# Kernel optimization log

Measured on AMD Instinct MI355X. Metric: run time of the kernel, lower is better.

Reference implementation:

```python
import jax, jax.numpy as jnp
import numpy as np

N = 50000          # nodes
E = 640000         # edges (before self-loops)
DIM_FEATS = 128
DIM_H = 32
HEADS1 = 8
NUM_CLASS = 16
NEG_SLOPE_ATT = 0.2   # PyG GATv2Conv default negative_slope
NEG_SLOPE_OUT = 0.01  # F.leaky_relu default


def setup_inputs() -> dict:
    key = jax.random.key(0)
    ks = jax.random.split(key, 12)
    s = 0.1
    x = jax.random.normal(ks[0], (N, DIM_FEATS), dtype=jnp.float32)
    edge_index = jax.random.randint(ks[1], (2, E), 0, N, dtype=jnp.int32)
    # GATv2Conv layer 1: dim_feats -> dim_h per head, 8 heads, concat
    W1l = jax.random.normal(ks[2], (DIM_FEATS, HEADS1 * DIM_H), dtype=jnp.float32) * s
    W1r = jax.random.normal(ks[3], (DIM_FEATS, HEADS1 * DIM_H), dtype=jnp.float32) * s
    att1 = jax.random.normal(ks[4], (HEADS1, DIM_H), dtype=jnp.float32) * s
    b1 = jnp.zeros((HEADS1 * DIM_H,), dtype=jnp.float32)
    # GATv2Conv layer 2: 256 -> num_class, 1 head, concat=False
    W2l = jax.random.normal(ks[5], (HEADS1 * DIM_H, NUM_CLASS), dtype=jnp.float32) * s
    W2r = jax.random.normal(ks[6], (HEADS1 * DIM_H, NUM_CLASS), dtype=jnp.float32) * s
    att2 = jax.random.normal(ks[7], (1, NUM_CLASS), dtype=jnp.float32) * s
    b2 = jnp.zeros((NUM_CLASS,), dtype=jnp.float32)
    return {"x": x, "edge_index": edge_index, "W1l": W1l, "W1r": W1r,
            "att1": att1, "b1": b1, "W2l": W2l, "W2r": W2r,
            "att2": att2, "b2": b2}


def _segment_softmax(scores, seg, num_segments):
    # scores: [E, H], seg: [E] destination node ids
    m = jax.ops.segment_max(scores, seg, num_segments=num_segments)  # [N, H]
    e = jnp.exp(scores - m[seg])
    denom = jax.ops.segment_sum(e, seg, num_segments=num_segments)   # [N, H]
    return e / (denom[seg] + 1e-16)


def _gatv2_layer(x, src, dst, Wl, Wr, att, bias, heads, out_ch, concat):
    n = x.shape[0]
    xl = (x @ Wl).reshape(n, heads, out_ch)  # source transform
    xr = (x @ Wr).reshape(n, heads, out_ch)  # target transform
    # per-edge GATv2 score: a^T LeakyReLU(xl[j] + xr[i])
    e = jax.nn.leaky_relu(xl[src] + xr[dst], negative_slope=NEG_SLOPE_ATT)  # [E,H,F]
    alpha = jnp.einsum('ehf,hf->eh', e, att)                                # [E,H]
    alpha = _segment_softmax(alpha, dst, n)
    msg = xl[src] * alpha[:, :, None]                                       # [E,H,F]
    out = jax.ops.segment_sum(msg, dst, num_segments=n)                     # [N,H,F]
    out = out.reshape(n, heads * out_ch) if concat else out.mean(axis=1)
    return out + bias


def reference(x, edge_index, W1l, W1r, att1, b1, W2l, W2r, att2, b2):
    # add_self_loops=True (PyG GATv2Conv default)
    loop = jnp.arange(N, dtype=edge_index.dtype)
    src = jnp.concatenate([edge_index[0], loop])
    dst = jnp.concatenate([edge_index[1], loop])
    # eval mode: all dropouts are identity
    h = _gatv2_layer(x, src, dst, W1l, W1r, att1, b1, HEADS1, DIM_H, concat=True)
    h = jax.nn.elu(h)
    h = _gatv2_layer(h, src, dst, W2l, W2r, att2, b2, 1, NUM_CLASS, concat=False)
    return jax.nn.leaky_relu(h, negative_slope=NEG_SLOPE_OUT)
```

## Files before the change

### kernel.cpp

```cpp
#include <hip/hip_runtime.h>
#include <math.h>

#define NN 50000
#define E0 640000
#define ET 690000
#define F1 128
#define D1 256
#define C2 16
#define NB 196
#define MPAD 50048
#define PADK 136
#define PADK2 264
#define LOG2E 1.4426950408889634f
#define NBK1 782

typedef _Float16 f16x8 __attribute__((ext_vector_type(8)));
typedef _Float16 h2 __attribute__((ext_vector_type(2)));
typedef __attribute__((ext_vector_type(4))) float f32x4;

__device__ __forceinline__ unsigned short f2h(float f) {
  union { _Float16 h; unsigned short u; } c;
  c.h = (_Float16)f;
  return c.u;
}
__device__ __forceinline__ float h2f(unsigned short u) {
  union { unsigned short u; _Float16 h; } c; c.u = u; return (float)c.h;
}
__device__ __forceinline__ h2 u2h2(unsigned u) {
  union { unsigned u; h2 h; } c; c.u = u; return c.h;
}
__device__ __forceinline__ unsigned h22u(h2 h) {
  union { h2 h; unsigned u; } c; c.h = h; return c.u;
}

__global__ __launch_bounds__(256) void k_prep(
    const float* __restrict__ x, const float* __restrict__ Wl,
    const float* __restrict__ Wr, const float* __restrict__ W2l,
    const float* __restrict__ W2r, const int* __restrict__ ei,
    unsigned short* __restrict__ xb, unsigned short* __restrict__ wt,
    unsigned short* __restrict__ wt2, int* __restrict__ deg) {
  const int b = blockIdx.x;
  if (b < 6256) {
    long long i = (long long)(b * 256 + threadIdx.x) * 4;
    if (i >= (long long)MPAD * F1) return;
    float4 v = (i < (long long)NN * F1) ? *(const float4*)&x[i]
                                        : make_float4(0.f, 0.f, 0.f, 0.f);
    ushort4 o;
    o.x = f2h(v.x); o.y = f2h(v.y); o.z = f2h(v.z); o.w = f2h(v.w);
    *(ushort4*)&xb[i] = o;
  } else if (b < 6512) {
    int tid = (b - 6256) * 256 + threadIdx.x;
    int n = tid >> 7, k = tid & 127;
    float v = (n < 256) ? Wl[k * 256 + n] : Wr[k * 256 + (n - 256)];
    wt[tid] = f2h(v);
  } else if (b < 6544) {
    int tid = (b - 6512) * 256 + threadIdx.x;
    int n = tid >> 8, k = tid & 255;
    float v = (n < 16) ? W2l[k * 16 + n] : W2r[k * 16 + (n - 16)];
    wt2[tid] = f2h(v);
  } else {
    int e = (b - 6544) * 256 + threadIdx.x;
    if (e >= ET) return;
    int d = (e < E0) ? ei[E0 + e] : (e - E0);
    atomicAdd(&deg[d], 1);
  }
}

__global__ __launch_bounds__(256) void k_gemm1m(
    const unsigned short* __restrict__ xb, const unsigned short* __restrict__ wt,
    unsigned short* __restrict__ xlh, unsigned short* __restrict__ xrh) {
  __shared__ unsigned short Al[128 * PADK];
  __shared__ unsigned short Bl[128 * PADK];
  const int t = threadIdx.x;
  const int m0 = blockIdx.x * 128;
  const int n0 = blockIdx.y * 128;
  {
    const int r = t >> 4;
    const int c = (t & 15) * 8;
#pragma unroll
    for (int p = 0; p < 8; ++p) {
      const int row = r + p * 16;
      *(float4*)&Al[row * PADK + c] = *(const float4*)&xb[(size_t)(m0 + row) * F1 + c];
      *(float4*)&Bl[row * PADK + c] = *(const float4*)&wt[(size_t)(n0 + row) * F1 + c];
    }
  }
  __syncthreads();
  const int wave = t >> 6, lane = t & 63;
  const int mw = (wave >> 1) * 64, nw = (wave & 1) * 64;
  const int fr = lane & 15, fq = lane >> 4;
  f32x4 acc[4][4] = {};
#pragma unroll
  for (int ks = 0; ks < 4; ++ks) {
    const int ko = ks * 32 + fq * 8;
    f16x8 a[4], b[4];
#pragma unroll
    for (int i = 0; i < 4; ++i)
      a[i] = *(const f16x8*)&Al[(mw + i * 16 + fr) * PADK + ko];
#pragma unroll
    for (int j = 0; j < 4; ++j)
      b[j] = *(const f16x8*)&Bl[(nw + j * 16 + fr) * PADK + ko];
#pragma unroll
    for (int i = 0; i < 4; ++i)
#pragma unroll
      for (int j = 0; j < 4; ++j)
        acc[i][j] = __builtin_amdgcn_mfma_f32_16x16x32_f16(a[i], b[j], acc[i][j], 0, 0, 0);
  }
  unsigned short* outp = (n0 < 256) ? xlh : xrh;
  const int cb = (n0 & 255) + nw + fr;
#pragma unroll
  for (int j = 0; j < 4; ++j) {
    const int col = cb + j * 16;
    const int head = col >> 5, f = col & 31;
    unsigned short* hp = outp + (size_t)head * NN * 32 + f;
#pragma unroll
    for (int i = 0; i < 4; ++i) {
      const int gm0 = m0 + mw + i * 16 + fq * 4;
#pragma unroll
      for (int r = 0; r < 4; ++r) {
        const int gm = gm0 + r;
        if (gm < NN) hp[(size_t)gm * 32] = f2h(acc[i][j][r]);
      }
    }
  }
}

__global__ __launch_bounds__(256) void k_scan_part(const int* __restrict__ deg,
                                                   int* __restrict__ part) {
  int i = blockIdx.x * 256 + threadIdx.x;
  int v = (i < NN) ? deg[i] : 0;
  v += __shfl_xor(v, 1);  v += __shfl_xor(v, 2);  v += __shfl_xor(v, 4);
  v += __shfl_xor(v, 8);  v += __shfl_xor(v, 16); v += __shfl_xor(v, 32);
  __shared__ int w[4];
  if ((threadIdx.x & 63) == 0) w[threadIdx.x >> 6] = v;
  __syncthreads();
  if (threadIdx.x == 0) part[blockIdx.x] = w[0] + w[1] + w[2] + w[3];
}

__global__ __launch_bounds__(256) void k_scan_top(int* __restrict__ part,
                                                  int* __restrict__ offs) {
  __shared__ int lds[256];
  int t = threadIdx.x;
  int v = (t < NB) ? part[t] : 0;
  lds[t] = v;
  __syncthreads();
  for (int off = 1; off < 256; off <<= 1) {
    int u = (t >= off) ? lds[t - off] : 0;
    __syncthreads();
    lds[t] += u;
    __syncthreads();
  }
  if (t < NB) part[t] = lds[t] - v;
  if (t == 255) offs[NN] = lds[255];
}

__global__ __launch_bounds__(256) void k_scan_apply(int* __restrict__ deg,
                                                    const int* __restrict__ part,
                                                    int* __restrict__ offs) {
  __shared__ int lds[256];
  int t = threadIdx.x;
  int i = blockIdx.x * 256 + t;
  int v = (i < NN) ? deg[i] : 0;
  lds[t] = v;
  __syncthreads();
  for (int off = 1; off < 256; off <<= 1) {
    int u = (t >= off) ? lds[t - off] : 0;
    __syncthreads();
    lds[t] += u;
    __syncthreads();
  }
  int excl = lds[t] - v + part[blockIdx.x];
  if (i < NN) { offs[i] = excl; deg[i] = excl; }
}

__global__ void k_scatter(const int* __restrict__ ei, int* __restrict__ cur,
                          unsigned short* __restrict__ csr) {
  int e = blockIdx.x * 256 + threadIdx.x;
  if (e >= ET) return;
  int s, d;
  if (e < E0) { s = ei[e]; d = ei[E0 + e]; } else { s = d = e - E0; }
  int pos = atomicAdd(&cur[d], 1);
  csr[pos] = (unsigned short)s;
}

__global__ __launch_bounds__(256) void k_agg1(
    const unsigned short* __restrict__ xlh, const unsigned short* __restrict__ xrh,
    unsigned short* __restrict__ hb,
    const int* __restrict__ offs, const unsigned short* __restrict__ csr,
    const float* __restrict__ att, const float* __restrict__ b1) {
  const int b = blockIdx.x;
  const int head = b & 7;
  const int wave = threadIdx.x >> 6;
  const int lane = threadIdx.x & 63;
  const int g = lane >> 2;
  const int j4 = lane & 3;
  const int n = (b >> 3) * 64 + wave * 16 + g;
  const bool valid = n < NN;
  const int colh = j4 * 8;
  const int col = head * 32 + colh;
  const unsigned short* xlhead = xlh + (size_t)head * NN * 32;

  const int nc = valid ? n : 0;
  const uint4 xru = *(const uint4*)&xrh[((size_t)head * NN + nc) * 32 + colh];
  h2 xr2[4];
  xr2[0] = u2h2(xru.x); xr2[1] = u2h2(xru.y);
  xr2[2] = u2h2(xru.z); xr2[3] = u2h2(xru.w);
  float at8[8];
  *(float4*)&at8[0] = *(const float4*)&att[col];
  *(float4*)&at8[4] = *(const float4*)&att[col + 4];
  h2 ath6[4], ath4[4];
#pragma unroll
  for (int j = 0; j < 4; ++j) {
    ath6[j] = h2{(_Float16)(at8[2 * j] * (0.6f * LOG2E)),
                 (_Float16)(at8[2 * j + 1] * (0.6f * LOG2E))};
    ath4[j] = h2{(_Float16)(at8[2 * j] * (0.4f * LOG2E)),
                 (_Float16)(at8[2 * j + 1] * (0.4f * LOG2E))};
  }
  float l = 0.f;
  h2 acc2[4] = {h2{0, 0}, h2{0, 0}, h2{0, 0}, h2{0, 0}};
  const int beg = valid ? offs[n] : 0;
  const int fin = valid ? offs[n + 1] : 0;

  auto score = [&](const h2* xh) -> float {
    float cv = 0.f, ca = 0.f;
#pragma unroll
    for (int j = 0; j < 4; ++j) {
      h2 v = xh[j] + xr2[j];
      h2 a = u2h2(h22u(v) & 0x7FFF7FFFu);
      cv = __builtin_amdgcn_fdot2(v, ath6[j], cv, false);
      ca = __builtin_amdgcn_fdot2(a, ath4[j], ca, false);
    }
    float c = cv + ca;
    c += __shfl_xor(c, 1);
    c += __shfl_xor(c, 2);
    return c;
  };

  int idx = beg;
  for (; idx + 1 < fin; idx += 2) {
    const int s0 = csr[idx], s1 = csr[idx + 1];
    const uint4 w0 = *(const uint4*)&xlhead[(size_t)s0 * 32 + colh];
    const uint4 w1 = *(const uint4*)&xlhead[(size_t)s1 * 32 + colh];
    h2 xh0[4], xh1[4];
    xh0[0] = u2h2(w0.x); xh0[1] = u2h2(w0.y); xh0[2] = u2h2(w0.z); xh0[3] = u2h2(w0.w);
    xh1[0] = u2h2(w1.x); xh1[1] = u2h2(w1.y); xh1[2] = u2h2(w1.z); xh1[3] = u2h2(w1.w);
    const float c0 = score(xh0);
    const float c1 = score(xh1);
    const float p0 = exp2f(c0), p1 = exp2f(c1);
    l += p0 + p1;
    const _Float16 p0h = (_Float16)p0, p1h = (_Float16)p1;
    const h2 p02 = h2{p0h, p0h}, p12 = h2{p1h, p1h};
#pragma unroll
    for (int j = 0; j < 4; ++j) acc2[j] += p02 * xh0[j] + p12 * xh1[j];
  }
  if (idx < fin) {
    const int s0 = csr[idx];
    const uint4 w0 = *(const uint4*)&xlhead[(size_t)s0 * 32 + colh];
    h2 xh0[4];
    xh0[0] = u2h2(w0.x); xh0[1] = u2h2(w0.y); xh0[2] = u2h2(w0.z); xh0[3] = u2h2(w0.w);
    const float c0 = score(xh0);
    const float p0 = exp2f(c0);
    l += p0;
    const _Float16 p0h = (_Float16)p0;
    const h2 p02 = h2{p0h, p0h};
#pragma unroll
    for (int j = 0; j < 4; ++j) acc2[j] += p02 * xh0[j];
  }
  if (valid) {
    const float rl = 1.f / (l + 1e-16f);
    float b8[8], o[8];
    *(float4*)&b8[0] = *(const float4*)&b1[col];
    *(float4*)&b8[4] = *(const float4*)&b1[col + 4];
#pragma unroll
    for (int j = 0; j < 4; ++j) {
      o[2 * j]     = (float)acc2[j][0] * rl + b8[2 * j];
      o[2 * j + 1] = (float)acc2[j][1] * rl + b8[2 * j + 1];
    }
#pragma unroll
    for (int k = 0; k < 8; ++k) o[k] = o[k] > 0.f ? o[k] : expm1f(o[k]);
    ushort4 p;
    p.x = f2h(o[0]); p.y = f2h(o[1]); p.z = f2h(o[2]); p.w = f2h(o[3]);
    ushort4 q;
    q.x = f2h(o[4]); q.y = f2h(o[5]); q.z = f2h(o[6]); q.w = f2h(o[7]);
    uint4 packed;
    packed.x = *(unsigned*)&p.x; packed.y = *(unsigned*)&p.z;
    packed.z = *(unsigned*)&q.x; packed.w = *(unsigned*)&q.z;
    *(uint4*)&hb[(size_t)n * D1 + col] = packed;
  }
}

__global__ __launch_bounds__(256) void k_gemm2m(
    const unsigned short* __restrict__ hb, const unsigned short* __restrict__ wt2,
    unsigned short* __restrict__ h2lh, float* __restrict__ h2r) {
  __shared__ unsigned short Bl[32 * PADK2];
  const int t = threadIdx.x;
  {
    const int n = t >> 3, k0 = (t & 7) * 32;
#pragma unroll
    for (int j = 0; j < 4; ++j)
      *(uint4*)&Bl[n * PADK2 + k0 + j * 8] = *(const uint4*)&wt2[n * 256 + k0 + j * 8];
  }
  __syncthreads();
  const int wave = t >> 6, lane = t & 63;
  const int fr = lane & 15, fq = lane >> 4;
  const int m0 = blockIdx.x * 128 + wave * 32;
  f32x4 acc[2][2] = {};
#pragma unroll
  for (int ks = 0; ks < 8; ++ks) {
    const int ko = ks * 32 + fq * 8;
    f16x8 a[2], b[2];
#pragma unroll
    for (int i = 0; i < 2; ++i) {
      int row = m0 + i * 16 + fr; if (row >= NN) row = NN - 1;
      a[i] = *(const f16x8*)&hb[(size_t)row * D1 + ko];
    }
#pragma unroll
    for (int j = 0; j < 2; ++j)
      b[j] = *(const f16x8*)&Bl[(j * 16 + fr) * PADK2 + ko];
#pragma unroll
    for (int i = 0; i < 2; ++i)
#pragma unroll
      for (int j = 0; j < 2; ++j)
        acc[i][j] = __builtin_amdgcn_mfma_f32_16x16x32_f16(a[i], b[j], acc[i][j], 0, 0, 0);
  }
#pragma unroll
  for (int i = 0; i < 2; ++i) {
    const int gm0 = m0 + i * 16 + fq * 4;
#pragma unroll
    for (int r = 0; r < 4; ++r) {
      const int gm = gm0 + r;
      if (gm < NN) {
        h2lh[(size_t)gm * C2 + fr] = f2h(acc[i][0][r]);
        h2r[(size_t)gm * C2 + fr] = acc[i][1][r];
      }
    }
  }
}

__global__ __launch_bounds__(256) void k_agg2(
    const unsigned short* __restrict__ h2lh, const float* __restrict__ h2r,
    const int* __restrict__ offs, const unsigned short* __restrict__ csr,
    const float* __restrict__ att2, const float* __restrict__ b2,
    float* __restrict__ out) {
  const int wave = threadIdx.x >> 6;
  const int lane = threadIdx.x & 63;
  const int n = blockIdx.x * 4 + wave;
  if (n >= NN) return;
  const int c = lane & 15, g = lane >> 4;
  const float xr_v = h2r[(size_t)n * C2 + c];
  const float att_v = att2[c] * LOG2E;
  float l = 0.f, acc = 0.f;
  const int beg = offs[n], fin = offs[n + 1];
  for (int idx = beg + g; idx < fin; idx += 4) {
    int s = csr[idx];
    float xlv = h2f(h2lh[(size_t)s * C2 + c]);
    float v = xlv + xr_v;
    v = fmaxf(v, 0.2f * v);
    float sc0 = v * att_v;
    sc0 += __shfl_xor(sc0, 1);
    sc0 += __shfl_xor(sc0, 2);
    sc0 += __shfl_xor(sc0, 4);
    sc0 += __shfl_xor(sc0, 8);
    float p = exp2f(sc0);
    l += p;
    acc = fmaf(p, xlv, acc);
  }
  l += __shfl_xor(l, 16);   l += __shfl_xor(l, 32);
  acc += __shfl_xor(acc, 16); acc += __shfl_xor(acc, 32);
  float o = acc / (l + 1e-16f) + b2[c];
  o = o > 0.f ? o : 0.01f * o;
  if (lane < 16) out[(size_t)n * C2 + c] = o;
}

extern "C" void kernel_launch(void* const* d_in, const int* in_sizes, int n_in,
                              void* d_out, int out_size, void* d_ws, size_t ws_size,
                              hipStream_t stream) {
  const float* x    = (const float*)d_in[0];
  const int*   ei   = (const int*)d_in[1];
  const float* W1l  = (const float*)d_in[2];
  const float* W1r  = (const float*)d_in[3];
  const float* att1 = (const float*)d_in[4];
  const float* b1   = (const float*)d_in[5];
  const float* W2l  = (const float*)d_in[6];
  const float* W2r  = (const float*)d_in[7];
  const float* att2 = (const float*)d_in[8];
  const float* b2   = (const float*)d_in[9];
  float* out = (float*)d_out;

  unsigned short* xlh = (unsigned short*)d_ws;
  unsigned short* xrh = xlh + (size_t)NN * D1;
  unsigned short* hb  = xrh + (size_t)NN * D1;
  int* deg  = (int*)(hb + (size_t)NN * D1);
  int* offs = deg + NN;
  unsigned short* csr = (unsigned short*)(offs + NN + 1);
  int* part = (int*)(csr + ET + 2);
  unsigned short* xb = (unsigned short*)(part + NB);
  unsigned short* wt = xb + (size_t)MPAD * F1;
  unsigned short* wt2 = wt + 512 * F1;
  unsigned short* h2lh = xlh;
  float* h2r = (float*)(h2lh + (size_t)NN * C2);

  hipMemsetAsync(deg, 0, NN * sizeof(int), stream);
  k_prep<<<6544 + (ET + 255) / 256, 256, 0, stream>>>(
      x, W1l, W1r, W2l, W2r, ei, xb, wt, wt2, deg);
  k_gemm1m<<<dim3(MPAD / 128, 4), 256, 0, stream>>>(xb, wt, xlh, xrh);
  k_scan_part<<<NB, 256, 0, stream>>>(deg, part);
  k_scan_top<<<1, 256, 0, stream>>>(part, offs);
  k_scan_apply<<<NB, 256, 0, stream>>>(deg, part, offs);
  k_scatter<<<(ET + 255) / 256, 256, 0, stream>>>(ei, deg, csr);
  k_agg1<<<NBK1 * 8, 256, 0, stream>>>(xlh, xrh, hb, offs, csr, att1, b1);
  k_gemm2m<<<(NN + 127) / 128, 256, 0, stream>>>(hb, wt2, h2lh, h2r);
  k_agg2<<<NN / 4, 256, 0, stream>>>(h2lh, h2r, offs, csr, att2, b2, out);
}
```

Measured before the change: 271.9 us.

## Fuse CSR build into one persistent kernel with grid barriers, fold x cast into GEMM

After: 465.1 us. 1.71x slower.

```diff
diff --git a/kernel.cpp b/kernel.cpp
--- a/kernel.cpp
+++ b/kernel.cpp
@@ -7,12 +7,12 @@
 #define F1 128
 #define D1 256
 #define C2 16
-#define NB 196
 #define MPAD 50048
 #define PADK 136
-#define PADK2 264
 #define LOG2E 1.4426950408889634f
 #define NBK1 782
+#define CSRB 512
+#define CH 98
 
 typedef _Float16 f16x8 __attribute__((ext_vector_type(8)));
 typedef _Float16 h2 __attribute__((ext_vector_type(2)));
@@ -33,41 +33,84 @@
   union { h2 h; unsigned u; } c; c.h = h; return c.u;
 }
 
-__global__ __launch_bounds__(256) void k_prep(
-    const float* __restrict__ x, const float* __restrict__ Wl,
-    const float* __restrict__ Wr, const float* __restrict__ W2l,
-    const float* __restrict__ W2r, const int* __restrict__ ei,
-    unsigned short* __restrict__ xb, unsigned short* __restrict__ wt,
-    unsigned short* __restrict__ wt2, int* __restrict__ deg) {
-  const int b = blockIdx.x;
-  if (b < 6256) {
-    long long i = (long long)(b * 256 + threadIdx.x) * 4;
-    if (i >= (long long)MPAD * F1) return;
-    float4 v = (i < (long long)NN * F1) ? *(const float4*)&x[i]
-                                        : make_float4(0.f, 0.f, 0.f, 0.f);
-    ushort4 o;
-    o.x = f2h(v.x); o.y = f2h(v.y); o.z = f2h(v.z); o.w = f2h(v.w);
-    *(ushort4*)&xb[i] = o;
-  } else if (b < 6512) {
-    int tid = (b - 6256) * 256 + threadIdx.x;
-    int n = tid >> 7, k = tid & 127;
-    float v = (n < 256) ? Wl[k * 256 + n] : Wr[k * 256 + (n - 256)];
-    wt[tid] = f2h(v);
-  } else if (b < 6544) {
-    int tid = (b - 6512) * 256 + threadIdx.x;
-    int n = tid >> 8, k = tid & 255;
-    float v = (n < 16) ? W2l[k * 16 + n] : W2r[k * 16 + (n - 16)];
-    wt2[tid] = f2h(v);
-  } else {
-    int e = (b - 6544) * 256 + threadIdx.x;
-    if (e >= ET) return;
+__device__ __forceinline__ void gbar(int* bar, int target) {
+  __syncthreads();
+  if (threadIdx.x == 0) {
+    __threadfence();
+    atomicAdd(bar, 1);
+    while (__hip_atomic_load(bar, __ATOMIC_RELAXED, __HIP_MEMORY_SCOPE_AGENT) < target)
+      __builtin_amdgcn_s_sleep(1);
+  }
+  __syncthreads();
+  __threadfence();
+}
+
+__global__ __launch_bounds__(256) void k_csr(
+    const float* __restrict__ Wl, const float* __restrict__ Wr,
+    const float* __restrict__ W2l, const float* __restrict__ W2r,
+    const int* __restrict__ ei,
+    unsigned short* __restrict__ wt, unsigned short* __restrict__ wt2,
+    int* __restrict__ deg, int* __restrict__ offs,
+    unsigned short* __restrict__ csr, int* __restrict__ part,
+    int* __restrict__ bar) {
+  const int b = blockIdx.x, t = threadIdx.x;
+  const int gtid = b * 256 + t;
+  for (int i = gtid; i < 512 * 128 + 32 * 256; i += CSRB * 256) {
+    if (i < 512 * 128) {
+      int n = i >> 7, k = i & 127;
+      wt[i] = f2h((n < 256) ? Wl[k * 256 + n] : Wr[k * 256 + (n - 256)]);
+    } else {
+      int j = i - 512 * 128;
+      int n = j >> 8, k = j & 255;
+      wt2[j] = f2h((n < 16) ? W2l[k * 16 + n] : W2r[k * 16 + (n - 16)]);
+    }
+  }
+  for (int e = gtid; e < ET; e += CSRB * 256) {
     int d = (e < E0) ? ei[E0 + e] : (e - E0);
     atomicAdd(&deg[d], 1);
   }
+  gbar(bar, CSRB);
+  __shared__ int lds[128];
+  __shared__ int red[5];
+  const int base = b * CH;
+  const int i0 = base + t;
+  int v = (t < CH && i0 < NN) ? deg[i0] : 0;
+  if (t < 128) lds[t] = v;
+  __syncthreads();
+  for (int off = 1; off < 128; off <<= 1) {
+    int u = (t >= off && t < 128) ? lds[t - off] : 0;
+    __syncthreads();
+    if (t < 128) lds[t] += u;
+    __syncthreads();
+  }
+  const int sumb = lds[127];
+  if (t == 0) part[b] = sumb;
+  gbar(bar, 2 * CSRB);
+  int pp = 0;
+  for (int i = t; i < b; i += 256)
+    pp += __hip_atomic_load(&part[i], __ATOMIC_RELAXED, __HIP_MEMORY_SCOPE_AGENT);
+  pp += __shfl_xor(pp, 1);  pp += __shfl_xor(pp, 2);  pp += __shfl_xor(pp, 4);
+  pp += __shfl_xor(pp, 8);  pp += __shfl_xor(pp, 16); pp += __shfl_xor(pp, 32);
+  if ((t & 63) == 0) red[t >> 6] = pp;
+  __syncthreads();
+  const int prefix = red[0] + red[1] + red[2] + red[3];
+  if (t < CH && i0 < NN) {
+    int excl = prefix + lds[t] - v;
+    offs[i0] = excl;
+    deg[i0] = excl;
+  }
+  if (b == CSRB - 1 && t == 0) offs[NN] = prefix + sumb;
+  gbar(bar, 3 * CSRB);
+  for (int e = gtid; e < ET; e += CSRB * 256) {
+    int s, d;
+    if (e < E0) { s = ei[e]; d = ei[E0 + e]; } else { s = d = e - E0; }
+    int pos = atomicAdd(&deg[d], 1);
+    csr[pos] = (unsigned short)s;
+  }
 }
 
 __global__ __launch_bounds__(256) void k_gemm1m(
-    const unsigned short* __restrict__ xb, const unsigned short* __restrict__ wt,
+    const float* __restrict__ x, const unsigned short* __restrict__ wt,
     unsigned short* __restrict__ xlh, unsigned short* __restrict__ xrh) {
   __shared__ unsigned short Al[128 * PADK];
   __shared__ unsigned short Bl[128 * PADK];
@@ -80,7 +123,16 @@
 #pragma unroll
     for (int p = 0; p < 8; ++p) {
       const int row = r + p * 16;
-      *(float4*)&Al[row * PADK + c] = *(const float4*)&xb[(size_t)(m0 + row) * F1 + c];
+      const int rg = m0 + row;
+      const float* xp = &x[(size_t)(rg < NN ? rg : NN - 1) * F1 + c];
+      float4 lo = *(const float4*)xp;
+      float4 hi = *(const float4*)(xp + 4);
+      h2 q0 = h2{(_Float16)lo.x, (_Float16)lo.y};
+      h2 q1 = h2{(_Float16)lo.z, (_Float16)lo.w};
+      h2 q2 = h2{(_Float16)hi.x, (_Float16)hi.y};
+      h2 q3 = h2{(_Float16)hi.z, (_Float16)hi.w};
+      uint4 st; st.x = h22u(q0); st.y = h22u(q1); st.z = h22u(q2); st.w = h22u(q3);
+      *(uint4*)&Al[row * PADK + c] = st;
       *(float4*)&Bl[row * PADK + c] = *(const float4*)&wt[(size_t)(n0 + row) * F1 + c];
     }
   }
@@ -122,64 +174,6 @@
       }
     }
   }
-}
-
-__global__ __launch_bounds__(256) void k_scan_part(const int* __restrict__ deg,
-                                                   int* __restrict__ part) {
-  int i = blockIdx.x * 256 + threadIdx.x;
-  int v = (i < NN) ? deg[i] : 0;
-  v += __shfl_xor(v, 1);  v += __shfl_xor(v, 2);  v += __shfl_xor(v, 4);
-  v += __shfl_xor(v, 8);  v += __shfl_xor(v, 16); v += __shfl_xor(v, 32);
-  __shared__ int w[4];
-  if ((threadIdx.x & 63) == 0) w[threadIdx.x >> 6] = v;
-  __syncthreads();
-  if (threadIdx.x == 0) part[blockIdx.x] = w[0] + w[1] + w[2] + w[3];
-}
-
-__global__ __launch_bounds__(256) void k_scan_top(int* __restrict__ part,
-                                                  int* __restrict__ offs) {
-  __shared__ int lds[256];
-  int t = threadIdx.x;
-  int v = (t < NB) ? part[t] : 0;
-  lds[t] = v;
-  __syncthreads();
-  for (int off = 1; off < 256; off <<= 1) {
-    int u = (t >= off) ? lds[t - off] : 0;
-    __syncthreads();
-    lds[t] += u;
-    __syncthreads();
-  }
-  if (t < NB) part[t] = lds[t] - v;
-  if (t == 255) offs[NN] = lds[255];
-}
-
-__global__ __launch_bounds__(256) void k_scan_apply(int* __restrict__ deg,
-                                                    const int* __restrict__ part,
-                                                    int* __restrict__ offs) {
-  __shared__ int lds[256];
-  int t = threadIdx.x;
-  int i = blockIdx.x * 256 + t;
-  int v = (i < NN) ? deg[i] : 0;
-  lds[t] = v;
-  __syncthreads();
-  for (int off = 1; off < 256; off <<= 1) {
-    int u = (t >= off) ? lds[t - off] : 0;
-    __syncthreads();
-    lds[t] += u;
-    __syncthreads();
-  }
-  int excl = lds[t] - v + part[blockIdx.x];
-  if (i < NN) { offs[i] = excl; deg[i] = excl; }
-}
-
-__global__ void k_scatter(const int* __restrict__ ei, int* __restrict__ cur,
-                          unsigned short* __restrict__ csr) {
-  int e = blockIdx.x * 256 + threadIdx.x;
-  if (e >= ET) return;
-  int s, d;
-  if (e < E0) { s = ei[e]; d = ei[E0 + e]; } else { s = d = e - E0; }
-  int pos = atomicAdd(&cur[d], 1);
-  csr[pos] = (unsigned short)s;
 }
 
 __global__ __launch_bounds__(256) void k_agg1(
@@ -291,15 +285,7 @@
 __global__ __launch_bounds__(256) void k_gemm2m(
     const unsigned short* __restrict__ hb, const unsigned short* __restrict__ wt2,
     unsigned short* __restrict__ h2lh, float* __restrict__ h2r) {
-  __shared__ unsigned short Bl[32 * PADK2];
   const int t = threadIdx.x;
-  {
-    const int n = t >> 3, k0 = (t & 7) * 32;
-#pragma unroll
-    for (int j = 0; j < 4; ++j)
-      *(uint4*)&Bl[n * PADK2 + k0 + j * 8] = *(const uint4*)&wt2[n * 256 + k0 + j * 8];
-  }
-  __syncthreads();
   const int wave = t >> 6, lane = t & 63;
   const int fr = lane & 15, fq = lane >> 4;
   const int m0 = blockIdx.x * 128 + wave * 32;
@@ -315,7 +301,7 @@
     }
 #pragma unroll
     for (int j = 0; j < 2; ++j)
-      b[j] = *(const f16x8*)&Bl[(j * 16 + fr) * PADK2 + ko];
+      b[j] = *(const f16x8*)&wt2[(j * 16 + fr) * 256 + ko];
 #pragma unroll
     for (int i = 0; i < 2; ++i)
 #pragma unroll
@@ -390,23 +376,19 @@
   unsigned short* xrh = xlh + (size_t)NN * D1;
   unsigned short* hb  = xrh + (size_t)NN * D1;
   int* deg  = (int*)(hb + (size_t)NN * D1);
-  int* offs = deg + NN;
+  int* part = deg + NN;
+  int* bar  = part + CSRB;
+  int* offs = bar + 1;
   unsigned short* csr = (unsigned short*)(offs + NN + 1);
-  int* part = (int*)(csr + ET + 2);
-  unsigned short* xb = (unsigned short*)(part + NB);
-  unsigned short* wt = xb + (size_t)MPAD * F1;
+  unsigned short* wt  = csr + ET + 2;
   unsigned short* wt2 = wt + 512 * F1;
   unsigned short* h2lh = xlh;
   float* h2r = (float*)(h2lh + (size_t)NN * C2);
 
-  hipMemsetAsync(deg, 0, NN * sizeof(int), stream);
-  k_prep<<<6544 + (ET + 255) / 256, 256, 0, stream>>>(
-      x, W1l, W1r, W2l, W2r, ei, xb, wt, wt2, deg);
-  k_gemm1m<<<dim3(MPAD / 128, 4), 256, 0, stream>>>(xb, wt, xlh, xrh);
-  k_scan_part<<<NB, 256, 0, stream>>>(deg, part);
-  k_scan_top<<<1, 256, 0, stream>>>(part, offs);
-  k_scan_apply<<<NB, 256, 0, stream>>>(deg, part, offs);
-  k_scatter<<<(ET + 255) / 256, 256, 0, stream>>>(ei, deg, csr);
+  hipMemsetAsync(deg, 0, (NN + CSRB + 1) * sizeof(int), stream);
+  k_csr<<<CSRB, 256, 0, stream>>>(W1l, W1r, W2l, W2r, ei, wt, wt2,
+                                  deg, offs, csr, part, bar);
+  k_gemm1m<<<dim3(MPAD / 128, 4), 256, 0, stream>>>(x, wt, xlh, xrh);
   k_agg1<<<NBK1 * 8, 256, 0, stream>>>(xlh, xrh, hb, offs, csr, att1, b1);
   k_gemm2m<<<(NN + 127) / 128, 256, 0, stream>>>(hb, wt2, h2lh, h2r);
   k_agg2<<<NN / 4, 256, 0, stream>>>(h2lh, h2r, offs, csr, att2, b2, out);
```

## Fuse x fp16 conversion into GEMM1, drop scan_top kernel and gemm2 LDS staging

Applied to the files above, without the earlier changes.

After: 270.2 us. Within noise of the previous version (-0.6%).

```diff
diff --git a/kernel.cpp b/kernel.cpp
--- a/kernel.cpp
+++ b/kernel.cpp
@@ -10,7 +10,6 @@
 #define NB 196
 #define MPAD 50048
 #define PADK 136
-#define PADK2 264
 #define LOG2E 1.4426950408889634f
 #define NBK1 782
 
@@ -34,32 +33,24 @@
 }
 
 __global__ __launch_bounds__(256) void k_prep(
-    const float* __restrict__ x, const float* __restrict__ Wl,
-    const float* __restrict__ Wr, const float* __restrict__ W2l,
-    const float* __restrict__ W2r, const int* __restrict__ ei,
-    unsigned short* __restrict__ xb, unsigned short* __restrict__ wt,
-    unsigned short* __restrict__ wt2, int* __restrict__ deg) {
+    const float* __restrict__ Wl, const float* __restrict__ Wr,
+    const float* __restrict__ W2l, const float* __restrict__ W2r,
+    const int* __restrict__ ei,
+    unsigned short* __restrict__ wt, unsigned short* __restrict__ wt2,
+    int* __restrict__ deg) {
   const int b = blockIdx.x;
-  if (b < 6256) {
-    long long i = (long long)(b * 256 + threadIdx.x) * 4;
-    if (i >= (long long)MPAD * F1) return;
-    float4 v = (i < (long long)NN * F1) ? *(const float4*)&x[i]
-                                        : make_float4(0.f, 0.f, 0.f, 0.f);
-    ushort4 o;
-    o.x = f2h(v.x); o.y = f2h(v.y); o.z = f2h(v.z); o.w = f2h(v.w);
-    *(ushort4*)&xb[i] = o;
-  } else if (b < 6512) {
-    int tid = (b - 6256) * 256 + threadIdx.x;
+  if (b < 256) {
+    int tid = b * 256 + threadIdx.x;
     int n = tid >> 7, k = tid & 127;
     float v = (n < 256) ? Wl[k * 256 + n] : Wr[k * 256 + (n - 256)];
     wt[tid] = f2h(v);
-  } else if (b < 6544) {
-    int tid = (b - 6512) * 256 + threadIdx.x;
+  } else if (b < 288) {
+    int tid = (b - 256) * 256 + threadIdx.x;
     int n = tid >> 8, k = tid & 255;
     float v = (n < 16) ? W2l[k * 16 + n] : W2r[k * 16 + (n - 16)];
     wt2[tid] = f2h(v);
   } else {
-    int e = (b - 6544) * 256 + threadIdx.x;
+    int e = (b - 288) * 256 + threadIdx.x;
     if (e >= ET) return;
     int d = (e < E0) ? ei[E0 + e] : (e - E0);
     atomicAdd(&deg[d], 1);
@@ -67,7 +58,7 @@
 }
 
 __global__ __launch_bounds__(256) void k_gemm1m(
-    const unsigned short* __restrict__ xb, const unsigned short* __restrict__ wt,
+    const float* __restrict__ x, const unsigned short* __restrict__ wt,
     unsigned short* __restrict__ xlh, unsigned short* __restrict__ xrh) {
   __shared__ unsigned short Al[128 * PADK];
   __shared__ unsigned short Bl[128 * PADK];
@@ -80,7 +71,16 @@
 #pragma unroll
     for (int p = 0; p < 8; ++p) {
       const int row = r + p * 16;
-      *(float4*)&Al[row * PADK + c] = *(const float4*)&xb[(size_t)(m0 + row) * F1 + c];
+      const int rg = m0 + row;
+      const float* xp = &x[(size_t)(rg < NN ? rg : NN - 1) * F1 + c];
+      float4 lo = *(const float4*)xp;
+      float4 hi = *(const float4*)(xp + 4);
+      h2 q0 = h2{(_Float16)lo.x, (_Float16)lo.y};
+      h2 q1 = h2{(_Float16)lo.z, (_Float16)lo.w};
+      h2 q2 = h2{(_Float16)hi.x, (_Float16)hi.y};
+      h2 q3 = h2{(_Float16)hi.z, (_Float16)hi.w};
+      uint4 st; st.x = h22u(q0); st.y = h22u(q1); st.z = h22u(q2); st.w = h22u(q3);
+      *(uint4*)&Al[row * PADK + c] = st;
       *(float4*)&Bl[row * PADK + c] = *(const float4*)&wt[(size_t)(n0 + row) * F1 + c];
     }
   }
@@ -136,40 +136,31 @@
   if (threadIdx.x == 0) part[blockIdx.x] = w[0] + w[1] + w[2] + w[3];
 }
 
-__global__ __launch_bounds__(256) void k_scan_top(int* __restrict__ part,
-                                                  int* __restrict__ offs) {
+__global__ __launch_bounds__(256) void k_scan_apply(int* __restrict__ deg,
+                                                    const int* __restrict__ part,
+                                                    int* __restrict__ offs) {
   __shared__ int lds[256];
-  int t = threadIdx.x;
-  int v = (t < NB) ? part[t] : 0;
+  __shared__ int red[4];
+  const int b = blockIdx.x, t = threadIdx.x;
+  const int i = b * 256 + t;
+  int v = (i < NN) ? deg[i] : 0;
   lds[t] = v;
+  int pp = 0;
+  for (int j = t; j < b; j += 256) pp += part[j];
+  pp += __shfl_xor(pp, 1);  pp += __shfl_xor(pp, 2);  pp += __shfl_xor(pp, 4);
+  pp += __shfl_xor(pp, 8);  pp += __shfl_xor(pp, 16); pp += __shfl_xor(pp, 32);
+  if ((t & 63) == 0) red[t >> 6] = pp;
   __syncthreads();
+  const int prefix = red[0] + red[1] + red[2] + red[3];
   for (int off = 1; off < 256; off <<= 1) {
     int u = (t >= off) ? lds[t - off] : 0;
     __syncthreads();
     lds[t] += u;
     __syncthreads();
   }
-  if (t < NB) part[t] = lds[t] - v;
-  if (t == 255) offs[NN] = lds[255];
-}
-
-__global__ __launch_bounds__(256) void k_scan_apply(int* __restrict__ deg,
-                                                    const int* __restrict__ part,
-                                                    int* __restrict__ offs) {
-  __shared__ int lds[256];
-  int t = threadIdx.x;
-  int i = blockIdx.x * 256 + t;
-  int v = (i < NN) ? deg[i] : 0;
-  lds[t] = v;
-  __syncthreads();
-  for (int off = 1; off < 256; off <<= 1) {
-    int u = (t >= off) ? lds[t - off] : 0;
-    __syncthreads();
-    lds[t] += u;
-    __syncthreads();
-  }
-  int excl = lds[t] - v + part[blockIdx.x];
+  int excl = prefix + lds[t] - v;
   if (i < NN) { offs[i] = excl; deg[i] = excl; }
+  if (b == NB - 1 && t == 255) offs[NN] = prefix + lds[255];
 }
 
 __global__ void k_scatter(const int* __restrict__ ei, int* __restrict__ cur,
@@ -291,15 +282,7 @@
 __global__ __launch_bounds__(256) void k_gemm2m(
     const unsigned short* __restrict__ hb, const unsigned short* __restrict__ wt2,
     unsigned short* __restrict__ h2lh, float* __restrict__ h2r) {
-  __shared__ unsigned short Bl[32 * PADK2];
   const int t = threadIdx.x;
-  {
-    const int n = t >> 3, k0 = (t & 7) * 32;
-#pragma unroll
-    for (int j = 0; j < 4; ++j)
-      *(uint4*)&Bl[n * PADK2 + k0 + j * 8] = *(const uint4*)&wt2[n * 256 + k0 + j * 8];
-  }
-  __syncthreads();
   const int wave = t >> 6, lane = t & 63;
   const int fr = lane & 15, fq = lane >> 4;
   const int m0 = blockIdx.x * 128 + wave * 32;
@@ -315,7 +298,7 @@
     }
 #pragma unroll
     for (int j = 0; j < 2; ++j)
-      b[j] = *(const f16x8*)&Bl[(j * 16 + fr) * PADK2 + ko];
+      b[j] = *(const f16x8*)&wt2[(j * 16 + fr) * 256 + ko];
 #pragma unroll
     for (int i = 0; i < 2; ++i)
 #pragma unroll
@@ -390,21 +373,19 @@
   unsigned short* xrh = xlh + (size_t)NN * D1;
   unsigned short* hb  = xrh + (size_t)NN * D1;
   int* deg  = (int*)(hb + (size_t)NN * D1);
-  int* offs = deg + NN;
+  int* part = deg + NN;
+  int* offs = part + NB;
   unsigned short* csr = (unsigned short*)(offs + NN + 1);
-  int* part = (int*)(csr + ET + 2);
-  unsigned short* xb = (unsigned short*)(part + NB);
-  unsigned short* wt = xb + (size_t)MPAD * F1;
+  unsigned short* wt  = csr + ET + 2;
   unsigned short* wt2 = wt + 512 * F1;
   unsigned short* h2lh = xlh;
   float* h2r = (float*)(h2lh + (size_t)NN * C2);
 
   hipMemsetAsync(deg, 0, NN * sizeof(int), stream);
-  k_prep<<<6544 + (ET + 255) / 256, 256, 0, stream>>>(
-      x, W1l, W1r, W2l, W2r, ei, xb, wt, wt2, deg);
-  k_gemm1m<<<dim3(MPAD / 128, 4), 256, 0, stream>>>(xb, wt, xlh, xrh);
+  k_prep<<<288 + (ET + 255) / 256, 256, 0, stream>>>(
+      W1l, W1r, W2l, W2r, ei, wt, wt2, deg);
+  k_gemm1m<<<dim3(MPAD / 128, 4), 256, 0, stream>>>(x, wt, xlh, xrh);
   k_scan_part<<<NB, 256, 0, stream>>>(deg, part);
-  k_scan_top<<<1, 256, 0, stream>>>(part, offs);
   k_scan_apply<<<NB, 256, 0, stream>>>(deg, part, offs);
   k_scatter<<<(ET + 255) / 256, 256, 0, stream>>>(ei, deg, csr);
   k_agg1<<<NBK1 * 8, 256, 0, stream>>>(xlh, xrh, hb, offs, csr, att1, b1);
```
